# Optimization experiments

Measured on AMD Instinct MI355X. Metric: run time of the kernel, lower is better.

Reference implementation:

```python
import jax, jax.numpy as jnp
import numpy as np

COMMIT_BETA = 0.25  # standard commitment-loss weight
EPS = 1e-10


def _vq_layer(x, codebook):
    """One VectorQuantize layer.
    x: [N, D] float32, codebook: [K, D] float32.
    Returns (quantized_st [N,D], indices [N], loss [1], perplexity scalar).
    """
    d = (jnp.sum(x * x, axis=1, keepdims=True)
         + jnp.sum(codebook * codebook, axis=1)[None, :]
         - 2.0 * (x @ codebook.T))
    indices = jnp.argmin(d, axis=1)                      # [N]
    quantized = codebook[indices]                        # gather [N, D]

    sg = jax.lax.stop_gradient
    codebook_loss = jnp.mean((sg(x) - quantized) ** 2)
    commit_loss = jnp.mean((x - sg(quantized)) ** 2)
    loss = (codebook_loss + COMMIT_BETA * commit_loss).reshape(1)

    # codebook usage perplexity: exp(-sum p log p) over empirical code probs
    K = codebook.shape[0]
    counts = jnp.zeros((K,), x.dtype).at[indices].add(1.0)
    probs = counts / x.shape[0]
    perplexity = jnp.exp(-jnp.sum(probs * jnp.log(probs + EPS)))

    # straight-through estimator
    quantized_st = x + sg(quantized - x)
    return quantized_st, indices, loss, perplexity


def setup_inputs() -> dict:
    key = jax.random.key(0)
    ks = jax.random.split(key, 5)
    N, D = 131072, 128
    cb_sizes = [1024, 1024, 512, 512]
    x = jax.random.normal(ks[0], (N, D), dtype=jnp.float32)
    cbs = {f"cb{i}": jax.random.normal(ks[i + 1], (k, D), dtype=jnp.float32)
           for i, k in enumerate(cb_sizes)}
    return {"x": x, **cbs}


def reference(x, cb0, cb1, cb2, cb3):
    codebooks = (cb0, cb1, cb2, cb3)
    quantized_out = jnp.zeros_like(x)
    residual = x
    idx_list, loss_list, perp_list, mse_list = [], [], [], []
    for cb in codebooks:  # fixed small number of structurally distinct layers
        quantized, indices, loss, perplexity = _vq_layer(residual, cb)
        residual = residual - quantized
        quantized_out = quantized_out + quantized
        idx_list.append(indices)
        loss_list.append(loss)
        perp_list.append(perplexity)
        mse_list.append(jnp.mean((x - quantized_out) ** 2))
    indices_cat = jnp.stack(idx_list, axis=1)        # [N, num_quantizers]
    loss_cat = jnp.concatenate(loss_list, axis=0)    # [num_quantizers]
    perplexity_cat = jnp.stack(perp_list, axis=0)    # [num_quantizers]
    return (quantized_out, indices_cat, loss_cat, perplexity_cat, tuple(mse_list))
```

## Files before the change

kernel.cpp:

```cpp
#include <hip/hip_runtime.h>
#include <math.h>


#define N_ROWS 131072
#define DDIM 128
#define BN 128
#define NTHREADS 256

#define OQ 0
#define OI 16777216
#define OL 17301504
#define OP 17301508
#define OM 17301512

#define RESCUE_EPS 1e-3f

typedef _Float16 f16x8 __attribute__((ext_vector_type(8)));
typedef float f32x4 __attribute__((ext_vector_type(4)));

__device__ __forceinline__ void gl16(const _Float16* g, _Float16* l) {
    __builtin_amdgcn_global_load_lds((const __attribute__((address_space(1))) void*)g,
                                     (__attribute__((address_space(3))) void*)l, 16, 0, 0);
}

__global__ void split_cb_kernel(const float* __restrict__ cb,
                                _Float16* __restrict__ out, int K)
{
    const int idx = blockIdx.x * 256 + threadIdx.x;
    const int col = idx >> 7, d = idx & 127;
    const float v = cb[idx];
    const _Float16 h = (_Float16)v;
    const _Float16 l = (_Float16)(v - (float)h);
    const int c = col >> 6, nf = (col >> 4) & 3, trow = col & 15;
    const int ks = d >> 5, kg = (d >> 3) & 3, i = d & 7;
    const size_t off = (size_t)(c * 4 + ks) * 4096 + nf * 512 + (kg * 16 + trow) * 8 + i;
    out[off] = h;
    out[off + 2048] = l;
}

__global__ void cbnorm_kernel(const float* __restrict__ cb,
                              float* __restrict__ norms, int K)
{
    const int row  = blockIdx.x * 4 + (threadIdx.x >> 6);
    const int lane = threadIdx.x & 63;
    const float2 v = *(const float2*)(cb + (size_t)row * DDIM + lane * 2);
    float s = fmaf(v.x, v.x, v.y * v.y);
#pragma unroll
    for (int o = 32; o; o >>= 1) s += __shfl_xor(s, o);
    if (lane == 0) norms[row] = s;
}

template<bool LAST>
__global__ __launch_bounds__(256, 2)
void vq_layer_kernel(const float* __restrict__ res_in,
                     const float* __restrict__ cb,
                     const _Float16* __restrict__ cbS,
                     const float* __restrict__ cbnorm,
                     const int K,
                     const float* __restrict__ x,
                     float* res_out,
                     float* __restrict__ idx_out,
                     const int layer,
                     int* __restrict__ hist,
                     float* __restrict__ sumsq)
{
    __shared__ _Float16 Bs[2][4096];
    __shared__ int   kw[BN];
    __shared__ int   rlist[BN];
    __shared__ int   nresc;
    __shared__ float wsum[4];

    const int tid  = threadIdx.x;
    const int w    = tid >> 6;
    const int wl   = tid & 63;
    const int trow = tid & 15;
    const int tkg  = (tid >> 4) & 3;
    const int n0   = blockIdx.x * BN;

    if (tid == 0) nresc = 0;

    f16x8 Ah[2][4], Al[2][4];
#pragma unroll
    for (int mf = 0; mf < 2; ++mf) {
        const int row = n0 + w * 32 + mf * 16 + trow;
        const float* rp = res_in + (size_t)row * DDIM;
#pragma unroll
        for (int ks = 0; ks < 4; ++ks) {
            const int d0 = ks * 32 + tkg * 8;
            const float4 f0 = *(const float4*)(rp + d0);
            const float4 f1 = *(const float4*)(rp + d0 + 4);
            const float vv[8] = {f0.x, f0.y, f0.z, f0.w, f1.x, f1.y, f1.z, f1.w};
#pragma unroll
            for (int i = 0; i < 8; ++i) {
                const _Float16 h = (_Float16)vv[i];
                Ah[mf][ks][i] = h;
                Al[mf][ks][i] = (_Float16)(vv[i] - (float)h);
            }
        }
    }

    {
        _Float16* dst = &Bs[0][w * 1024];
        const _Float16* src = cbS + (size_t)w * 1024 + wl * 8;
        gl16(src, dst);
        gl16(src + 512, dst + 512);
    }
    __syncthreads();

    float m1v[8], m2v[8];
    int   m1k[8];
#pragma unroll
    for (int i = 0; i < 8; ++i) { m1v[i] = 3.4e38f; m2v[i] = 3.4e38f; m1k[i] = 0x7fffffff; }

    const int nchunks = K >> 6;
    const int nslices = nchunks * 4;

    for (int c = 0; c < nchunks; ++c) {
        f32x4 acc[2][4];
#pragma unroll
        for (int mf = 0; mf < 2; ++mf)
#pragma unroll
            for (int nf = 0; nf < 4; ++nf) acc[mf][nf] = f32x4{0.f, 0.f, 0.f, 0.f};

#pragma unroll
        for (int ks = 0; ks < 4; ++ks) {
            const int s = c * 4 + ks;
            const int cur = s & 1;
            if (s + 1 < nslices) {
                _Float16* dst = &Bs[cur ^ 1][w * 1024];
                const _Float16* src = cbS + (size_t)(s + 1) * 4096 + w * 1024 + wl * 8;
                gl16(src, dst);
                gl16(src + 512, dst + 512);
            }
#pragma unroll
            for (int nf = 0; nf < 4; ++nf) {
                const f16x8 bh = *(const f16x8*)&Bs[cur][nf * 512 + wl * 8];
                const f16x8 bl = *(const f16x8*)&Bs[cur][2048 + nf * 512 + wl * 8];
#pragma unroll
                for (int mf = 0; mf < 2; ++mf) {
                    acc[mf][nf] = __builtin_amdgcn_mfma_f32_16x16x32_f16(Ah[mf][ks], bh, acc[mf][nf], 0, 0, 0);
                    acc[mf][nf] = __builtin_amdgcn_mfma_f32_16x16x32_f16(Al[mf][ks], bh, acc[mf][nf], 0, 0, 0);
                    acc[mf][nf] = __builtin_amdgcn_mfma_f32_16x16x32_f16(Ah[mf][ks], bl, acc[mf][nf], 0, 0, 0);
                }
            }
            __syncthreads();
        }

#pragma unroll
        for (int nf = 0; nf < 4; ++nf) {
            const int col = c * 64 + nf * 16 + trow;
            const float nvv = cbnorm[col];
#pragma unroll
            for (int mf = 0; mf < 2; ++mf) {
#pragma unroll
                for (int r = 0; r < 4; ++r) {
                    const float dv = fmaf(-2.f, acc[mf][nf][r], nvv);
                    const int t8 = mf * 4 + r;
                    if (dv < m1v[t8]) { m2v[t8] = m1v[t8]; m1v[t8] = dv; m1k[t8] = col; }
                    else if (dv < m2v[t8]) m2v[t8] = dv;
                }
            }
        }
    }

#pragma unroll
    for (int t8 = 0; t8 < 8; ++t8) {
        float v1 = m1v[t8], v2 = m2v[t8];
        int   k1 = m1k[t8];
#pragma unroll
        for (int off = 1; off < 16; off <<= 1) {
            const float ov1 = __shfl_xor(v1, off);
            const int   ok1 = __shfl_xor(k1, off);
            const float ov2 = __shfl_xor(v2, off);
            const bool take = (ov1 < v1) || (ov1 == v1 && ok1 < k1);
            const float nm2 = take ? fminf(v1, ov2) : fminf(ov1, v2);
            if (take) { v1 = ov1; k1 = ok1; }
            v2 = nm2;
        }
        if (trow == 0) {
            const int lrow = w * 32 + (t8 >> 2) * 16 + tkg * 4 + (t8 & 3);
            kw[lrow] = k1;
            if (v2 - v1 < RESCUE_EPS) {
                const int p = atomicAdd(&nresc, 1);
                rlist[p] = lrow;
            }
        }
    }
    __syncthreads();

    const int nr = nresc;
    for (int j = w; j < nr; j += 4) {
        const int lrow = rlist[j];
        const float* rp = res_in + (size_t)(n0 + lrow) * DDIM;
        float best = 3.4e38f; int bestk = 0x7fffffff;
        for (int kk = wl; kk < K; kk += 64) {
            const float* ep = cb + (size_t)kk * DDIM;
            float dot = 0.f;
#pragma unroll 8
            for (int d = 0; d < DDIM; d += 4) {
                const float4 rv = *(const float4*)(rp + d);
                const float4 ev = *(const float4*)(ep + d);
                dot = fmaf(rv.x, ev.x, dot); dot = fmaf(rv.y, ev.y, dot);
                dot = fmaf(rv.z, ev.z, dot); dot = fmaf(rv.w, ev.w, dot);
            }
            const float dv = fmaf(-2.f, dot, cbnorm[kk]);
            if (dv < best) { best = dv; bestk = kk; }
        }
#pragma unroll
        for (int off = 1; off < 64; off <<= 1) {
            const float ov = __shfl_xor(best, off);
            const int   ok = __shfl_xor(bestk, off);
            if (ov < best || (ov == best && ok < bestk)) { best = ov; bestk = ok; }
        }
        if (wl == 0) kw[lrow] = bestk;
    }
    __syncthreads();

    if (tid < BN) {
        const int bk = kw[tid];
        idx_out[(size_t)(n0 + tid) * 4 + layer] = (float)bk;
        atomicAdd(&hist[bk], 1);
    }

    float ssum = 0.f;
#pragma unroll
    for (int v = 0; v < 16; ++v) {
        const int flat = (v * NTHREADS + tid) * 4;
        const int r  = flat >> 7;
        const int d0 = flat & 127;
        const int k  = kw[r];
        const float4 e  = *(const float4*)(cb + (size_t)k * DDIM + d0);
        const float4 rs = *(const float4*)(res_in + (size_t)(n0 + r) * DDIM + d0);
        float4 rn;
        rn.x = rs.x - (rs.x + (e.x - rs.x));
        rn.y = rs.y - (rs.y + (e.y - rs.y));
        rn.z = rs.z - (rs.z + (e.z - rs.z));
        rn.w = rs.w - (rs.w + (e.w - rs.w));
        if (LAST) {
            const float4 xv = *(const float4*)(x + (size_t)(n0 + r) * DDIM + d0);
            float4 q;
            q.x = xv.x - rn.x; q.y = xv.y - rn.y; q.z = xv.z - rn.z; q.w = xv.w - rn.w;
            *(float4*)(res_out + (size_t)(n0 + r) * DDIM + d0) = q;
        } else {
            *(float4*)(res_out + (size_t)(n0 + r) * DDIM + d0) = rn;
        }
        ssum += rn.x * rn.x + rn.y * rn.y + rn.z * rn.z + rn.w * rn.w;
    }
#pragma unroll
    for (int o = 32; o; o >>= 1) ssum += __shfl_xor(ssum, o);
    if (wl == 0) wsum[w] = ssum;
    __syncthreads();
    if (tid == 0) atomicAdd(&sumsq[layer], wsum[0] + wsum[1] + wsum[2] + wsum[3]);
}

__global__ void finalize_kernel(const int* __restrict__ hist,
                                const float* __restrict__ sumsq,
                                float* __restrict__ out)
{
    const int l   = blockIdx.x;
    const int K   = (l < 2) ? 1024 : 512;
    const int off = (l < 2) ? l * 1024 : 2048 + (l - 2) * 512;
    const int tid = threadIdx.x;
    float local = 0.f;
    for (int k = tid; k < K; k += 256) {
        const float p = (float)hist[off + k] * (1.0f / 131072.0f);
        local += p * logf(p + 1e-10f);
    }
#pragma unroll
    for (int o = 32; o; o >>= 1) local += __shfl_xor(local, o);
    __shared__ float w[4];
    if ((tid & 63) == 0) w[tid >> 6] = local;
    __syncthreads();
    if (tid == 0) {
        const float H = w[0] + w[1] + w[2] + w[3];
        out[OP + l] = expf(-H);
        const float mse = sumsq[l] * (1.0f / (131072.0f * 128.0f));
        out[OM + l] = mse;
        out[OL + l] = 1.25f * mse;
    }
}

extern "C" void kernel_launch(void* const* d_in, const int* in_sizes, int n_in,
                              void* d_out, int out_size, void* d_ws, size_t ws_size,
                              hipStream_t stream)
{
    const float* x = (const float*)d_in[0];
    const float* cbs[4] = {(const float*)d_in[1], (const float*)d_in[2],
                           (const float*)d_in[3], (const float*)d_in[4]};
    const int Ks[4]       = {1024, 1024, 512, 512};
    const int normoff[4]  = {0, 1024, 2048, 2560};
    const size_t cbSoff[4] = {0, 262144, 524288, 655360};

    float* out  = (float*)d_out;
    float* qres = out + OQ;
    float* idxf = out + OI;

    int*      hist  = (int*)d_ws;
    float*    sumsq = (float*)d_ws + 3072;
    float*    norms = (float*)d_ws + 3076;
    _Float16* cbS   = (_Float16*)((float*)d_ws + 6148);

    hipMemsetAsync(d_ws, 0, (3072 + 4) * sizeof(int), stream);

    for (int c = 0; c < 4; ++c) {
        split_cb_kernel<<<(Ks[c] * 128) / 256, 256, 0, stream>>>(cbs[c], cbS + cbSoff[c], Ks[c]);
        cbnorm_kernel<<<Ks[c] / 4, 256, 0, stream>>>(cbs[c], norms + normoff[c], Ks[c]);
    }

    const int grid = N_ROWS / BN;
    vq_layer_kernel<false><<<grid, NTHREADS, 0, stream>>>(
        x,    cbs[0], cbS + cbSoff[0], norms + normoff[0], Ks[0], nullptr,
        qres, idxf, 0, hist + normoff[0], sumsq);
    vq_layer_kernel<false><<<grid, NTHREADS, 0, stream>>>(
        qres, cbs[1], cbS + cbSoff[1], norms + normoff[1], Ks[1], nullptr,
        qres, idxf, 1, hist + normoff[1], sumsq);
    vq_layer_kernel<false><<<grid, NTHREADS, 0, stream>>>(
        qres, cbs[2], cbS + cbSoff[2], norms + normoff[2], Ks[2], nullptr,
        qres, idxf, 2, hist + normoff[2], sumsq);
    vq_layer_kernel<true><<<grid, NTHREADS, 0, stream>>>(
        qres, cbs[3], cbS + cbSoff[3], norms + normoff[3], Ks[3], x,
        qres, idxf, 3, hist + normoff[3], sumsq);

    finalize_kernel<<<4, 256, 0, stream>>>(hist, sumsq, out);
}
```

Baseline: 954.6 us.

## Double block rows to 256 and stage whole 64-column codebook chunks per barrier

Each block now covers 256 rows with 512 threads (8 waves), so every codebook tile in LDS is reused across twice as many rows. Codebook prefetch moves from per-32-wide k-slice to per-64-column chunk, covering all four k-slices, which cuts barriers from four per chunk to one. LDS grows to about 66 KB of dynamic shared memory, and launch bounds of 512 threads with 4 blocks per CU put more pressure on registers and occupancy. The risks are register spilling under the tighter bound and fewer resident blocks per CU.

```diff
diff --git a/kernel.cpp b/kernel.cpp
--- a/kernel.cpp
+++ b/kernel.cpp
@@ -4,8 +4,8 @@
 
 #define N_ROWS 131072
 #define DDIM 128
-#define BN 128
-#define NTHREADS 256
+#define BN 256
+#define NTHREADS 512
 
 #define OQ 0
 #define OI 16777216
@@ -33,7 +33,7 @@
     const _Float16 l = (_Float16)(v - (float)h);
     const int c = col >> 6, nf = (col >> 4) & 3, trow = col & 15;
     const int ks = d >> 5, kg = (d >> 3) & 3, i = d & 7;
-    const size_t off = (size_t)(c * 4 + ks) * 4096 + nf * 512 + (kg * 16 + trow) * 8 + i;
+    const size_t off = (size_t)c * 16384 + ks * 4096 + nf * 512 + (kg * 16 + trow) * 8 + i;
     out[off] = h;
     out[off + 2048] = l;
 }
@@ -51,7 +51,7 @@
 }
 
 template<bool LAST>
-__global__ __launch_bounds__(256, 2)
+__global__ __launch_bounds__(512, 4)
 void vq_layer_kernel(const float* __restrict__ res_in,
                      const float* __restrict__ cb,
                      const _Float16* __restrict__ cbS,
@@ -64,11 +64,12 @@
                      int* __restrict__ hist,
                      float* __restrict__ sumsq)
 {
-    __shared__ _Float16 Bs[2][4096];
-    __shared__ int   kw[BN];
-    __shared__ int   rlist[BN];
-    __shared__ int   nresc;
-    __shared__ float wsum[4];
+    extern __shared__ char smem[];
+    _Float16* Bs   = (_Float16*)smem;
+    int*      kw   = (int*)(smem + 65536);
+    int*      rlist= (int*)(smem + 66560);
+    int*      nresc= (int*)(smem + 67584);
+    float*    wsum = (float*)(smem + 67600);
 
     const int tid  = threadIdx.x;
     const int w    = tid >> 6;
@@ -77,7 +78,7 @@
     const int tkg  = (tid >> 4) & 3;
     const int n0   = blockIdx.x * BN;
 
-    if (tid == 0) nresc = 0;
+    if (tid == 0) *nresc = 0;
 
     f16x8 Ah[2][4], Al[2][4];
 #pragma unroll
@@ -100,10 +101,11 @@
     }
 
     {
-        _Float16* dst = &Bs[0][w * 1024];
-        const _Float16* src = cbS + (size_t)w * 1024 + wl * 8;
-        gl16(src, dst);
-        gl16(src + 512, dst + 512);
+        const _Float16* src = cbS + w * 512 + wl * 8;
+        _Float16* dst = Bs + w * 512;
+#pragma unroll
+        for (int r = 0; r < 4; ++r)
+            gl16(src + r * 4096, dst + r * 4096);
     }
     __syncthreads();
 
@@ -113,29 +115,31 @@
     for (int i = 0; i < 8; ++i) { m1v[i] = 3.4e38f; m2v[i] = 3.4e38f; m1k[i] = 0x7fffffff; }
 
     const int nchunks = K >> 6;
-    const int nslices = nchunks * 4;
 
     for (int c = 0; c < nchunks; ++c) {
+        const int cur = c & 1;
+
+        if (c + 1 < nchunks) {
+            const _Float16* src = cbS + (size_t)(c + 1) * 16384 + w * 512 + wl * 8;
+            _Float16* dst = Bs + (cur ^ 1) * 16384 + w * 512;
+#pragma unroll
+            for (int r = 0; r < 4; ++r)
+                gl16(src + r * 4096, dst + r * 4096);
+        }
+
         f32x4 acc[2][4];
 #pragma unroll
         for (int mf = 0; mf < 2; ++mf)
 #pragma unroll
             for (int nf = 0; nf < 4; ++nf) acc[mf][nf] = f32x4{0.f, 0.f, 0.f, 0.f};
 
+        const _Float16* Bb = Bs + cur * 16384;
 #pragma unroll
         for (int ks = 0; ks < 4; ++ks) {
-            const int s = c * 4 + ks;
-            const int cur = s & 1;
-            if (s + 1 < nslices) {
-                _Float16* dst = &Bs[cur ^ 1][w * 1024];
-                const _Float16* src = cbS + (size_t)(s + 1) * 4096 + w * 1024 + wl * 8;
-                gl16(src, dst);
-                gl16(src + 512, dst + 512);
-            }
 #pragma unroll
             for (int nf = 0; nf < 4; ++nf) {
-                const f16x8 bh = *(const f16x8*)&Bs[cur][nf * 512 + wl * 8];
-                const f16x8 bl = *(const f16x8*)&Bs[cur][2048 + nf * 512 + wl * 8];
+                const f16x8 bh = *(const f16x8*)(Bb + ks * 4096 + nf * 512 + wl * 8);
+                const f16x8 bl = *(const f16x8*)(Bb + ks * 4096 + 2048 + nf * 512 + wl * 8);
 #pragma unroll
                 for (int mf = 0; mf < 2; ++mf) {
                     acc[mf][nf] = __builtin_amdgcn_mfma_f32_16x16x32_f16(Ah[mf][ks], bh, acc[mf][nf], 0, 0, 0);
@@ -143,7 +147,6 @@
                     acc[mf][nf] = __builtin_amdgcn_mfma_f32_16x16x32_f16(Ah[mf][ks], bl, acc[mf][nf], 0, 0, 0);
                 }
             }
-            __syncthreads();
         }
 
 #pragma unroll
@@ -161,6 +164,8 @@
                 }
             }
         }
+
+        __syncthreads();
     }
 
 #pragma unroll
@@ -181,15 +186,15 @@
             const int lrow = w * 32 + (t8 >> 2) * 16 + tkg * 4 + (t8 & 3);
             kw[lrow] = k1;
             if (v2 - v1 < RESCUE_EPS) {
-                const int p = atomicAdd(&nresc, 1);
+                const int p = atomicAdd(nresc, 1);
                 rlist[p] = lrow;
             }
         }
     }
     __syncthreads();
 
-    const int nr = nresc;
-    for (int j = w; j < nr; j += 4) {
+    const int nr = *nresc;
+    for (int j = w; j < nr; j += 8) {
         const int lrow = rlist[j];
         const float* rp = res_in + (size_t)(n0 + lrow) * DDIM;
         float best = 3.4e38f; int bestk = 0x7fffffff;
@@ -250,7 +255,12 @@
     for (int o = 32; o; o >>= 1) ssum += __shfl_xor(ssum, o);
     if (wl == 0) wsum[w] = ssum;
     __syncthreads();
-    if (tid == 0) atomicAdd(&sumsq[layer], wsum[0] + wsum[1] + wsum[2] + wsum[3]);
+    if (tid == 0) {
+        float t = 0.f;
+#pragma unroll
+        for (int i = 0; i < 8; ++i) t += wsum[i];
+        atomicAdd(&sumsq[layer], t);
+    }
 }
 
 __global__ void finalize_kernel(const int* __restrict__ hist,
@@ -300,6 +310,12 @@
     float*    norms = (float*)d_ws + 3076;
     _Float16* cbS   = (_Float16*)((float*)d_ws + 6148);
 
+    const int LDSB = 67648;
+    (void)hipFuncSetAttribute(reinterpret_cast<const void*>(&vq_layer_kernel<false>),
+                              hipFuncAttributeMaxDynamicSharedMemorySize, LDSB);
+    (void)hipFuncSetAttribute(reinterpret_cast<const void*>(&vq_layer_kernel<true>),
+                              hipFuncAttributeMaxDynamicSharedMemorySize, LDSB);
+
     hipMemsetAsync(d_ws, 0, (3072 + 4) * sizeof(int), stream);
 
     for (int c = 0; c < 4; ++c) {
@@ -308,16 +324,16 @@
     }
 
     const int grid = N_ROWS / BN;
-    vq_layer_kernel<false><<<grid, NTHREADS, 0, stream>>>(
+    vq_layer_kernel<false><<<grid, NTHREADS, LDSB, stream>>>(
         x,    cbs[0], cbS + cbSoff[0], norms + normoff[0], Ks[0], nullptr,
         qres, idxf, 0, hist + normoff[0], sumsq);
-    vq_layer_kernel<false><<<grid, NTHREADS, 0, stream>>>(
+    vq_layer_kernel<false><<<grid, NTHREADS, LDSB, stream>>>(
         qres, cbs[1], cbS + cbSoff[1], norms + normoff[1], Ks[1], nullptr,
         qres, idxf, 1, hist + normoff[1], sumsq);
-    vq_layer_kernel<false><<<grid, NTHREADS, 0, stream>>>(
+    vq_layer_kernel<false><<<grid, NTHREADS, LDSB, stream>>>(
         qres, cbs[2], cbS + cbSoff[2], norms + normoff[2], Ks[2], nullptr,
         qres, idxf, 2, hist + normoff[2], sumsq);
-    vq_layer_kernel<true><<<grid, NTHREADS, 0, stream>>>(
+    vq_layer_kernel<true><<<grid, NTHREADS, LDSB, stream>>>(
         qres, cbs[3], cbS + cbSoff[3], norms + normoff[3], Ks[3], x,
         qres, idxf, 3, hist + normoff[3], sumsq);
 
```

After: 778.7 us. -18.4%, faster.
